# Performance work log

Hardware: AMD Instinct MI355X
Metric: run time of the kernel (lower is better)

The kernel has to match this reference:

```python
import jax, jax.numpy as jnp
import numpy as np

EMBED_DIM = 1024
NUM_HEADS = 16
HEAD_DIM = EMBED_DIM // NUM_HEADS
B, S = 2, 2048


def setup_inputs() -> dict:
    key = jax.random.key(0)
    ks = jax.random.split(key, 11)
    f32 = jnp.float32
    return {
        "q": jax.random.normal(ks[0], (B, S, EMBED_DIM), f32),
        "k": jax.random.normal(ks[1], (B, S, EMBED_DIM), f32),
        "v": jax.random.normal(ks[2], (B, S, EMBED_DIM), f32),
        # per-head projection weights stacked over heads: [H, E, Dh]
        "Wq": jax.random.normal(ks[3], (NUM_HEADS, EMBED_DIM, HEAD_DIM), f32),
        "Wk": jax.random.normal(ks[4], (NUM_HEADS, EMBED_DIM, HEAD_DIM), f32),
        "Wv": jax.random.normal(ks[5], (NUM_HEADS, EMBED_DIM, HEAD_DIM), f32),
        "bq": jax.random.normal(ks[6], (NUM_HEADS, HEAD_DIM), f32),
        "bk": jax.random.normal(ks[7], (NUM_HEADS, HEAD_DIM), f32),
        "bv": jax.random.normal(ks[8], (NUM_HEADS, HEAD_DIM), f32),
        "Wo": jax.random.normal(ks[9], (EMBED_DIM, EMBED_DIM), f32),
        "bo": jax.random.normal(ks[10], (EMBED_DIM,), f32),
    }


def reference(q, k, v, Wq, Wk, Wv, bq, bk, bv, Wo, bo):
    scale = jnp.asarray(np.sqrt(HEAD_DIM), q.dtype)
    # batched per-head projections: [B,S,E] x [H,E,D] -> [B,H,S,D]
    Q = jnp.einsum("bse,hed->bhsd", q, Wq) + bq[None, :, None, :]
    K = jnp.einsum("bse,hed->bhsd", k, Wk) + bk[None, :, None, :]
    V = jnp.einsum("bse,hed->bhsd", v, Wv) + bv[None, :, None, :]
    # attention scores [B,H,S,S]; original applies mask to a discarded tensor,
    # so output is unmasked softmax(QK^T/scale) @ V
    att = jnp.einsum("bhsd,bhtd->bhst", Q, K) / scale
    att = jax.nn.softmax(att, axis=-1)
    ctx = jnp.einsum("bhst,bhtd->bhsd", att, V)  # [B,H,S,D]
    # concat heads (head order preserved) then output projection
    ctx = ctx.transpose(0, 2, 1, 3).reshape(ctx.shape[0], ctx.shape[2], -1)  # [B,S,E]
    return ctx @ Wo + bo
```

## Files before the change

kernel.cpp:

```cpp
#include <hip/hip_runtime.h>
#include <hip/hip_bf16.h>

typedef unsigned short u16;
typedef unsigned int   u32;
typedef _Float16 f16;
typedef __attribute__((ext_vector_type(4))) float f32x4;
typedef __attribute__((ext_vector_type(8))) short s16x8;
typedef __attribute__((ext_vector_type(8))) f16 f16x8;
typedef __attribute__((ext_vector_type(2))) __fp16 fp16x2;
typedef __attribute__((ext_vector_type(4))) u16 u16x4;
typedef __attribute__((ext_vector_type(2))) u32 u32x2;

#define DI __device__ __forceinline__

static constexpr int Bb = 2, Ss = 2048, Hh = 16, Dd = 64, Ee = 1024;
static constexpr int Mrows = Bb * Ss;
static constexpr size_t NE = (size_t)Mrows * Ee;
static constexpr size_t WN = (size_t)Ee * Ee;
static constexpr float QSCALE = 0.125f * 1.44269504088896f;

DI float bf2f(u16 h) { u32 u = ((u32)h) << 16; return __builtin_bit_cast(float, u); }
DI u16 f2bf(float f) {
    u32 u = __builtin_bit_cast(u32, f);
    u32 r = (u + 0x7FFFu + ((u >> 16) & 1u)) >> 16;
    return (u16)r;
}
DI u16 f2h(float f) { f16 h = (f16)f; return __builtin_bit_cast(u16, h); }
DI u32 pkrtz(float a, float b) {
    fp16x2 r = __builtin_amdgcn_cvt_pkrtz(a, b);
    return __builtin_bit_cast(u32, r);
}
DI float ex2(float x) { return __builtin_amdgcn_exp2f(x); }

#define MFMA_BF(a, b, c) __builtin_amdgcn_mfma_f32_16x16x32_bf16((a), (b), (c), 0, 0, 0)
#define MFMA_F16(a, b, c) __builtin_amdgcn_mfma_f32_16x16x32_f16( \
    __builtin_bit_cast(f16x8, (a)), __builtin_bit_cast(f16x8, (b)), (c), 0, 0, 0)

DI void gld16(const u16* g, u16* l) {
    __builtin_amdgcn_global_load_lds((const __attribute__((address_space(1))) void*)g,
                                     (__attribute__((address_space(3))) void*)l, 16, 0, 0);
}

__global__ __launch_bounds__(256) void k_split3(
    const float* __restrict__ q, const float* __restrict__ k, const float* __restrict__ v,
    u16* __restrict__ qh, u16* __restrict__ ql,
    u16* __restrict__ kh, u16* __restrict__ kl, u16* __restrict__ vh) {
    int i = blockIdx.x * 256 + threadIdx.x;
    int y = blockIdx.y;
    if (y == 2) { vh[i] = f2h(v[i]); return; }
    const float* s = y ? k : q;
    u16* h = y ? kh : qh;
    u16* l = y ? kl : ql;
    float val = s[i];
    u16 hh = f2bf(val);
    h[i] = hh;
    l[i] = f2bf(val - bf2f(hh));
}

__global__ __launch_bounds__(256) void k_wprep(
    const float* __restrict__ Wq, const float* __restrict__ Wk,
    const float* __restrict__ Wv, const float* __restrict__ Wo,
    u16* __restrict__ WqTh, u16* __restrict__ WqTl,
    u16* __restrict__ WkTh, u16* __restrict__ WkTl,
    u16* __restrict__ WvT, u16* __restrict__ WoT) {
    __shared__ float Ts[64 * 65];
    const int y = blockIdx.y;
    const int ti = blockIdx.x >> 4, tj = blockIdx.x & 15;
    const float* W = (y == 0) ? Wq : (y == 1) ? Wk : (y == 2) ? Wv : Wo;
    const int t = threadIdx.x;
    const int col = t & 63, rb = (t >> 6) * 16;
#pragma unroll
    for (int rr = 0; rr < 16; rr++) {
        int row = rb + rr;
        float v = (y < 3) ? W[(size_t)ti * 65536 + (size_t)(tj * 64 + row) * 64 + col]
                          : W[(size_t)(tj * 64 + row) * Ee + ti * 64 + col];
        Ts[row * 65 + col] = v;
    }
    __syncthreads();
#pragma unroll
    for (int rr = 0; rr < 16; rr++) {
        int orow = rb + rr;
        int ocol = col;
        float v = Ts[ocol * 65 + orow];
        size_t oidx = (size_t)(ti * 64 + orow) * Ee + tj * 64 + ocol;
        if (y == 0) {
            u16 hh = f2bf(v); WqTh[oidx] = hh; WqTl[oidx] = f2bf(v - bf2f(hh));
        } else if (y == 1) {
            u16 hh = f2bf(v); WkTh[oidx] = hh; WkTl[oidx] = f2bf(v - bf2f(hh));
        } else if (y == 2) {
            WvT[oidx] = f2h(v);
        } else {
            WoT[oidx] = f2h(v);
        }
    }
}

template <int SPLIT, int F16, int OUTMODE>
DI void gemm_body(const u16* __restrict__ Ah, const u16* __restrict__ Al,
                  const u16* __restrict__ Bh, const u16* __restrict__ Bl,
                  const float* __restrict__ bias,
                  u16* __restrict__ C16h, u16* __restrict__ C16l, float* __restrict__ Cf,
                  float scale, u16* As0, u16* As1, u16* Bs0, u16* Bs1) {
    constexpr int M = Mrows, N = Ee, K = Ee;
    const int tid = threadIdx.x;
    const int wave = tid >> 6, lane = tid & 63;
    const int quad = lane >> 4, l16 = lane & 15;
    const int m0 = blockIdx.y * 128, n0 = blockIdx.x * 128;
    const int wm = (wave >> 1) * 64, wn = (wave & 1) * 64;

    f32x4 acc[4][4];
#pragma unroll
    for (int i = 0; i < 4; i++)
#pragma unroll
        for (int j = 0; j < 4; j++) acc[i][j] = (f32x4)0.0f;

    for (int kk = 0; kk < K; kk += 32) {
        __syncthreads();
#pragma unroll
        for (int i = 0; i < 2; i++) {
            int c = tid + i * 256;
            int row = c >> 2, j = c & 3;
            size_t ga = (size_t)(m0 + row) * K + kk + j * 8;
            gld16(Ah + ga, As0 + c * 8);
            if constexpr (SPLIT) gld16(Al + ga, As1 + c * 8);
            size_t gb = (size_t)(n0 + row) * K + kk + j * 8;
            gld16(Bh + gb, Bs0 + c * 8);
            if constexpr (SPLIT) gld16(Bl + gb, Bs1 + c * 8);
        }
        __syncthreads();

        s16x8 bf[4][2];
#pragma unroll
        for (int nt = 0; nt < 4; nt++) {
            int r = wn + nt * 16 + l16;
            bf[nt][0] = *(const s16x8*)&Bs0[r * 32 + quad * 8];
            if constexpr (SPLIT) bf[nt][1] = *(const s16x8*)&Bs1[r * 32 + quad * 8];
        }
#pragma unroll
        for (int mt = 0; mt < 4; mt++) {
            int r = wm + mt * 16 + l16;
            s16x8 a0 = *(const s16x8*)&As0[r * 32 + quad * 8];
            s16x8 a1;
            if constexpr (SPLIT) a1 = *(const s16x8*)&As1[r * 32 + quad * 8];
#pragma unroll
            for (int nt = 0; nt < 4; nt++) {
                if constexpr (F16) {
                    acc[mt][nt] = MFMA_F16(a0, bf[nt][0], acc[mt][nt]);
                } else {
                    acc[mt][nt] = MFMA_BF(a0, bf[nt][0], acc[mt][nt]);
                    if constexpr (SPLIT) {
                        acc[mt][nt] = MFMA_BF(a0, bf[nt][1], acc[mt][nt]);
                        acc[mt][nt] = MFMA_BF(a1, bf[nt][0], acc[mt][nt]);
                    }
                }
            }
        }
    }

#pragma unroll
    for (int mt = 0; mt < 4; mt++)
#pragma unroll
        for (int nt = 0; nt < 4; nt++) {
            int gn = n0 + wn + nt * 16 + l16;
            float bs = bias[gn];
            if constexpr (OUTMODE == 1) {
                int gm = m0 + wm + mt * 16 + quad * 4;
                u16x4 pk;
#pragma unroll
                for (int r = 0; r < 4; r++) pk[r] = f2h((acc[mt][nt][r] + bs) * scale);
                *(u16x4*)&C16h[(size_t)gn * M + gm] = pk;
            } else {
#pragma unroll
                for (int r = 0; r < 4; r++) {
                    int gm = m0 + wm + mt * 16 + quad * 4 + r;
                    float v = (acc[mt][nt][r] + bs) * scale;
                    if constexpr (OUTMODE == 0) {
                        Cf[(size_t)gm * N + gn] = v;
                    } else {
                        u16 hh = f2bf(v);
                        C16h[(size_t)gm * N + gn] = hh;
                        C16l[(size_t)gm * N + gn] = f2bf(v - bf2f(hh));
                    }
                }
            }
        }
}

__global__ __launch_bounds__(256, 3) void k_qkv(
    const u16* __restrict__ qh, const u16* __restrict__ ql,
    const u16* __restrict__ kh, const u16* __restrict__ kl,
    const u16* __restrict__ vh,
    const u16* __restrict__ WqTh, const u16* __restrict__ WqTl,
    const u16* __restrict__ WkTh, const u16* __restrict__ WkTl,
    const u16* __restrict__ WvT,
    const float* __restrict__ bq, const float* __restrict__ bk, const float* __restrict__ bv,
    u16* __restrict__ Qh, u16* __restrict__ Ql2,
    u16* __restrict__ Kh, u16* __restrict__ Kl2, u16* __restrict__ Vt) {
    __shared__ u16 As[2][128 * 32];
    __shared__ u16 Bs[2][128 * 32];
    int z = blockIdx.z;
    if (z == 0)
        gemm_body<1, 0, 2>(qh, ql, WqTh, WqTl, bq, Qh, Ql2, nullptr, QSCALE,
                           As[0], As[1], Bs[0], Bs[1]);
    else if (z == 1)
        gemm_body<1, 0, 2>(kh, kl, WkTh, WkTl, bk, Kh, Kl2, nullptr, 1.0f,
                           As[0], As[1], Bs[0], Bs[1]);
    else
        gemm_body<0, 1, 1>(vh, nullptr, WvT, nullptr, bv, Vt, nullptr, nullptr, 1.0f,
                           As[0], As[1], Bs[0], Bs[1]);
}

__global__ __launch_bounds__(256, 3) void k_out(
    const u16* __restrict__ ctx, const u16* __restrict__ WoT,
    const float* __restrict__ bo, float* __restrict__ out) {
    __shared__ u16 As[128 * 32];
    __shared__ u16 Bs[128 * 32];
    gemm_body<0, 1, 0>(ctx, nullptr, WoT, nullptr, bo, nullptr, nullptr, out, 1.0f,
                       As, nullptr, Bs, nullptr);
}

__global__ __launch_bounds__(256, 2) void k_attn(
    const u16* __restrict__ Qh, const u16* __restrict__ Ql,
    const u16* __restrict__ Kh, const u16* __restrict__ Kl,
    const u16* __restrict__ Vt, u16* __restrict__ ctx) {
    const int bh = blockIdx.x;
    const int b = bh >> 4, h = bh & 15;
    const int q0 = blockIdx.y * 128;
    const int rowBase = b * Ss + q0;
    const int hc = h * 64;

    __shared__ u16 Ks[2][64 * 64];
    __shared__ u16 Vs[64 * 64];
    __shared__ u16 Pw[4][32 * 72];

    const int tid = threadIdx.x;
    const int wave = tid >> 6, lane = tid & 63;
    const int quad = lane >> 4, l16 = lane & 15;

    s16x8 bq[2][2][2];
#pragma unroll
    for (int nt = 0; nt < 2; nt++) {
        int row = rowBase + wave * 32 + nt * 16 + l16;
#pragma unroll
        for (int kc = 0; kc < 2; kc++) {
            bq[nt][kc][0] = *(const s16x8*)(Qh + (size_t)row * Ee + hc + kc * 32 + quad * 8);
            bq[nt][kc][1] = *(const s16x8*)(Ql + (size_t)row * Ee + hc + kc * 32 + quad * 8);
        }
    }

    f32x4 o[2][4];
#pragma unroll
    for (int nt = 0; nt < 2; nt++)
#pragma unroll
        for (int dg = 0; dg < 4; dg++) o[nt][dg] = (f32x4)0.0f;
    float m_[2] = {-1e30f, -1e30f};
    float l_[2] = {0.f, 0.f};

    for (int t0 = 0; t0 < Ss; t0 += 64) {
        const int kRowBase = b * Ss + t0;
        __syncthreads();
#pragma unroll
        for (int i = 0; i < 2; i++) {
            int c = tid + i * 256;
            int row = c >> 3, j = c & 7;
            int sj = j ^ (row & 7);
            *(s16x8*)&Ks[0][row * 64 + sj * 8] =
                *(const s16x8*)(Kh + (size_t)(kRowBase + row) * Ee + hc + j * 8);
            *(s16x8*)&Ks[1][row * 64 + sj * 8] =
                *(const s16x8*)(Kl + (size_t)(kRowBase + row) * Ee + hc + j * 8);
            *(s16x8*)&Vs[row * 64 + sj * 8] =
                *(const s16x8*)(Vt + (size_t)(hc + row) * Mrows + kRowBase + j * 8);
        }
        __syncthreads();

        f32x4 st[2][4];
#pragma unroll
        for (int nt = 0; nt < 2; nt++)
#pragma unroll
            for (int mt = 0; mt < 4; mt++) st[nt][mt] = (f32x4)0.0f;
#pragma unroll
        for (int mt = 0; mt < 4; mt++) {
            int tr = mt * 16 + l16;
#pragma unroll
            for (int kc = 0; kc < 2; kc++) {
                int sj = (kc * 4 + quad) ^ (l16 & 7);
                s16x8 akh = *(const s16x8*)&Ks[0][tr * 64 + sj * 8];
                s16x8 akl = *(const s16x8*)&Ks[1][tr * 64 + sj * 8];
#pragma unroll
                for (int nt = 0; nt < 2; nt++) {
                    st[nt][mt] = MFMA_BF(akh, bq[nt][kc][0], st[nt][mt]);
                    st[nt][mt] = MFMA_BF(akh, bq[nt][kc][1], st[nt][mt]);
                    st[nt][mt] = MFMA_BF(akl, bq[nt][kc][0], st[nt][mt]);
                }
            }
        }

#pragma unroll
        for (int nt = 0; nt < 2; nt++) {
            float t01 = fmaxf(fmaxf(st[nt][0][0], st[nt][0][1]), fmaxf(st[nt][0][2], st[nt][0][3]));
            float t23 = fmaxf(fmaxf(st[nt][1][0], st[nt][1][1]), fmaxf(st[nt][1][2], st[nt][1][3]));
            float t45 = fmaxf(fmaxf(st[nt][2][0], st[nt][2][1]), fmaxf(st[nt][2][2], st[nt][2][3]));
            float t67 = fmaxf(fmaxf(st[nt][3][0], st[nt][3][1]), fmaxf(st[nt][3][2], st[nt][3][3]));
            float tmax = fmaxf(fmaxf(t01, t23), fmaxf(t45, t67));
            tmax = fmaxf(tmax, __shfl_xor(tmax, 16));
            tmax = fmaxf(tmax, __shfl_xor(tmax, 32));
            float mnew = fmaxf(m_[nt], tmax);
            float al = ex2(m_[nt] - mnew);
            m_[nt] = mnew;
            float psum = 0.f;
#pragma unroll
            for (int mt = 0; mt < 4; mt++) {
                float p0 = ex2(st[nt][mt][0] - mnew);
                float p1 = ex2(st[nt][mt][1] - mnew);
                float p2 = ex2(st[nt][mt][2] - mnew);
                float p3 = ex2(st[nt][mt][3] - mnew);
                psum += (p0 + p1) + (p2 + p3);
                u32x2 pk;
                pk[0] = pkrtz(p0, p1);
                pk[1] = pkrtz(p2, p3);
                *(u32x2*)&Pw[wave][(nt * 16 + l16) * 72 + mt * 16 + quad * 4] = pk;
            }
            psum += __shfl_xor(psum, 16);
            psum += __shfl_xor(psum, 32);
            l_[nt] = l_[nt] * al + psum;
#pragma unroll
            for (int dg = 0; dg < 4; dg++) o[nt][dg] *= al;
        }

#pragma unroll
        for (int kc = 0; kc < 2; kc++) {
            s16x8 bp[2];
#pragma unroll
            for (int nt = 0; nt < 2; nt++)
                bp[nt] = *(const s16x8*)&Pw[wave][(nt * 16 + l16) * 72 + kc * 32 + quad * 8];
#pragma unroll
            for (int dg = 0; dg < 4; dg++) {
                int sj = (kc * 4 + quad) ^ (l16 & 7);
                s16x8 av = *(const s16x8*)&Vs[(dg * 16 + l16) * 64 + sj * 8];
#pragma unroll
                for (int nt = 0; nt < 2; nt++) o[nt][dg] = MFMA_F16(av, bp[nt], o[nt][dg]);
            }
        }
    }

#pragma unroll
    for (int nt = 0; nt < 2; nt++) {
        float inv = 1.0f / l_[nt];
        int gm = rowBase + wave * 32 + nt * 16 + l16;
#pragma unroll
        for (int dg = 0; dg < 4; dg++) {
            u32x2 pk;
            pk[0] = pkrtz(o[nt][dg][0] * inv, o[nt][dg][1] * inv);
            pk[1] = pkrtz(o[nt][dg][2] * inv, o[nt][dg][3] * inv);
            *(u32x2*)&ctx[(size_t)gm * Ee + hc + dg * 16 + quad * 4] = pk;
        }
    }
}

extern "C" void kernel_launch(void* const* d_in, const int* in_sizes, int n_in,
                              void* d_out, int out_size, void* d_ws, size_t ws_size,
                              hipStream_t stream) {
    const float* q   = (const float*)d_in[0];
    const float* kin = (const float*)d_in[1];
    const float* v   = (const float*)d_in[2];
    const float* Wq  = (const float*)d_in[3];
    const float* Wk  = (const float*)d_in[4];
    const float* Wv  = (const float*)d_in[5];
    const float* bq  = (const float*)d_in[6];
    const float* bk  = (const float*)d_in[7];
    const float* bv  = (const float*)d_in[8];
    const float* Wo  = (const float*)d_in[9];
    const float* bo  = (const float*)d_in[10];

    u16* ws = (u16*)d_ws;
    u16 *qh = ws,          *ql = ws + NE,     *kh = ws + 2 * NE, *kl = ws + 3 * NE;
    u16 *vh = ws + 4 * NE;
    u16 *Qh = ws + 5 * NE, *Ql = ws + 6 * NE, *Kh = ws + 7 * NE, *Kl = ws + 8 * NE;
    u16 *Vt = ws + 9 * NE, *ctx = ws + 10 * NE;
    u16 *WqTh = ws + 11 * NE;
    u16 *WqTl = WqTh + WN, *WkTh = WqTh + 2 * WN, *WkTl = WqTh + 3 * WN;
    u16 *WvT = WqTh + 4 * WN, *WoT = WqTh + 5 * WN;

    dim3 b256(256);
    k_split3<<<dim3(NE / 256, 3), b256, 0, stream>>>(q, kin, v, qh, ql, kh, kl, vh);
    k_wprep<<<dim3(256, 4), b256, 0, stream>>>(Wq, Wk, Wv, Wo,
                                               WqTh, WqTl, WkTh, WkTl, WvT, WoT);

    k_qkv<<<dim3(8, 32, 3), b256, 0, stream>>>(qh, ql, kh, kl, vh,
                                               WqTh, WqTl, WkTh, WkTl, WvT,
                                               bq, bk, bv, Qh, Ql, Kh, Kl, Vt);

    k_attn<<<dim3(Bb * Hh, Ss / 128), b256, 0, stream>>>(Qh, Ql, Kh, Kl, Vt, ctx);

    k_out<<<dim3(8, 32), b256, 0, stream>>>(ctx, WoT, bo, (float*)d_out);
}
```

Measured before the change: 296.3 us.

## Prefetch next K/V tile into registers during attention compute

The attention loop now issues the global loads for the next K/V tile into registers before computing the current tile, and writes them to shared memory only after the current tile's MFMAs finish. This hides global-load latency behind compute. The change also precomputes the swizzled LDS base pointers and raises wave priority around the MFMA sections with s_setprio. In exchange it needs extra registers for the six prefetched vectors, which could reduce occupancy under launch_bounds(256,2).

```diff
diff --git a/kernel.cpp b/kernel.cpp
--- a/kernel.cpp
+++ b/kernel.cpp
@@ -237,6 +237,40 @@
     const int wave = tid >> 6, lane = tid & 63;
     const int quad = lane >> 4, l16 = lane & 15;
 
+    const int c0 = tid, c1 = tid + 256;
+    const int srow0 = c0 >> 3, sgj0 = c0 & 7;
+    const int srow1 = c1 >> 3, sgj1 = c1 & 7;
+    const int soff0 = srow0 * 64 + (sgj0 ^ (srow0 & 7)) * 8;
+    const int soff1 = srow1 * 64 + (sgj1 ^ (srow1 & 7)) * 8;
+
+    s16x8 rkh0, rkh1, rkl0, rkl1, rv0, rv1;
+    auto loadT = [&](int t0) {
+        const int kRowBase = b * Ss + t0;
+        rkh0 = *(const s16x8*)(Kh + (size_t)(kRowBase + srow0) * Ee + hc + sgj0 * 8);
+        rkl0 = *(const s16x8*)(Kl + (size_t)(kRowBase + srow0) * Ee + hc + sgj0 * 8);
+        rv0  = *(const s16x8*)(Vt + (size_t)(hc + srow0) * Mrows + kRowBase + sgj0 * 8);
+        rkh1 = *(const s16x8*)(Kh + (size_t)(kRowBase + srow1) * Ee + hc + sgj1 * 8);
+        rkl1 = *(const s16x8*)(Kl + (size_t)(kRowBase + srow1) * Ee + hc + sgj1 * 8);
+        rv1  = *(const s16x8*)(Vt + (size_t)(hc + srow1) * Mrows + kRowBase + sgj1 * 8);
+    };
+    auto storeT = [&]() {
+        *(s16x8*)&Ks[0][soff0] = rkh0;
+        *(s16x8*)&Ks[0][soff1] = rkh1;
+        *(s16x8*)&Ks[1][soff0] = rkl0;
+        *(s16x8*)&Ks[1][soff1] = rkl1;
+        *(s16x8*)&Vs[soff0] = rv0;
+        *(s16x8*)&Vs[soff1] = rv1;
+    };
+
+    const int sw0 = ((0 * 4 + quad) ^ (l16 & 7)) * 8;
+    const int sw1 = ((1 * 4 + quad) ^ (l16 & 7)) * 8;
+    const u16* akb0 = &Ks[0][l16 * 64 + sw0];
+    const u16* akb1 = &Ks[0][l16 * 64 + sw1];
+    const u16* avb0 = &Vs[l16 * 64 + sw0];
+    const u16* avb1 = &Vs[l16 * 64 + sw1];
+    u16* pwb = &Pw[wave][l16 * 72 + quad * 4];
+    const u16* pbb = &Pw[wave][l16 * 72 + quad * 8];
+
     s16x8 bq[2][2][2];
 #pragma unroll
     for (int nt = 0; nt < 2; nt++) {
@@ -256,44 +290,37 @@
     float m_[2] = {-1e30f, -1e30f};
     float l_[2] = {0.f, 0.f};
 
+    loadT(0);
+    storeT();
+    __syncthreads();
+
     for (int t0 = 0; t0 < Ss; t0 += 64) {
-        const int kRowBase = b * Ss + t0;
-        __syncthreads();
-#pragma unroll
-        for (int i = 0; i < 2; i++) {
-            int c = tid + i * 256;
-            int row = c >> 3, j = c & 7;
-            int sj = j ^ (row & 7);
-            *(s16x8*)&Ks[0][row * 64 + sj * 8] =
-                *(const s16x8*)(Kh + (size_t)(kRowBase + row) * Ee + hc + j * 8);
-            *(s16x8*)&Ks[1][row * 64 + sj * 8] =
-                *(const s16x8*)(Kl + (size_t)(kRowBase + row) * Ee + hc + j * 8);
-            *(s16x8*)&Vs[row * 64 + sj * 8] =
-                *(const s16x8*)(Vt + (size_t)(hc + row) * Mrows + kRowBase + j * 8);
-        }
-        __syncthreads();
+        const bool more = (t0 + 64) < Ss;
+        if (more) loadT(t0 + 64);
 
         f32x4 st[2][4];
 #pragma unroll
         for (int nt = 0; nt < 2; nt++)
 #pragma unroll
             for (int mt = 0; mt < 4; mt++) st[nt][mt] = (f32x4)0.0f;
+        __builtin_amdgcn_s_setprio(1);
 #pragma unroll
         for (int mt = 0; mt < 4; mt++) {
-            int tr = mt * 16 + l16;
-#pragma unroll
-            for (int kc = 0; kc < 2; kc++) {
-                int sj = (kc * 4 + quad) ^ (l16 & 7);
-                s16x8 akh = *(const s16x8*)&Ks[0][tr * 64 + sj * 8];
-                s16x8 akl = *(const s16x8*)&Ks[1][tr * 64 + sj * 8];
-#pragma unroll
-                for (int nt = 0; nt < 2; nt++) {
-                    st[nt][mt] = MFMA_BF(akh, bq[nt][kc][0], st[nt][mt]);
-                    st[nt][mt] = MFMA_BF(akh, bq[nt][kc][1], st[nt][mt]);
-                    st[nt][mt] = MFMA_BF(akl, bq[nt][kc][0], st[nt][mt]);
-                }
+            s16x8 akh0 = *(const s16x8*)(akb0 + mt * 1024);
+            s16x8 akl0 = *(const s16x8*)(akb0 + mt * 1024 + 4096);
+            s16x8 akh1 = *(const s16x8*)(akb1 + mt * 1024);
+            s16x8 akl1 = *(const s16x8*)(akb1 + mt * 1024 + 4096);
+#pragma unroll
+            for (int nt = 0; nt < 2; nt++) {
+                st[nt][mt] = MFMA_BF(akh0, bq[nt][0][0], st[nt][mt]);
+                st[nt][mt] = MFMA_BF(akh0, bq[nt][0][1], st[nt][mt]);
+                st[nt][mt] = MFMA_BF(akl0, bq[nt][0][0], st[nt][mt]);
+                st[nt][mt] = MFMA_BF(akh1, bq[nt][1][0], st[nt][mt]);
+                st[nt][mt] = MFMA_BF(akh1, bq[nt][1][1], st[nt][mt]);
+                st[nt][mt] = MFMA_BF(akl1, bq[nt][1][0], st[nt][mt]);
             }
         }
+        __builtin_amdgcn_s_setprio(0);
 
 #pragma unroll
         for (int nt = 0; nt < 2; nt++) {
@@ -318,7 +345,7 @@
                 u32x2 pk;
                 pk[0] = pkrtz(p0, p1);
                 pk[1] = pkrtz(p2, p3);
-                *(u32x2*)&Pw[wave][(nt * 16 + l16) * 72 + mt * 16 + quad * 4] = pk;
+                *(u32x2*)(pwb + nt * 1152 + mt * 16) = pk;
             }
             psum += __shfl_xor(psum, 16);
             psum += __shfl_xor(psum, 32);
@@ -327,19 +354,27 @@
             for (int dg = 0; dg < 4; dg++) o[nt][dg] *= al;
         }
 
+        __builtin_amdgcn_s_setprio(1);
 #pragma unroll
         for (int kc = 0; kc < 2; kc++) {
             s16x8 bp[2];
 #pragma unroll
             for (int nt = 0; nt < 2; nt++)
-                bp[nt] = *(const s16x8*)&Pw[wave][(nt * 16 + l16) * 72 + kc * 32 + quad * 8];
+                bp[nt] = *(const s16x8*)(pbb + nt * 1152 + kc * 32);
+            const u16* avb = kc ? avb1 : avb0;
 #pragma unroll
             for (int dg = 0; dg < 4; dg++) {
-                int sj = (kc * 4 + quad) ^ (l16 & 7);
-                s16x8 av = *(const s16x8*)&Vs[(dg * 16 + l16) * 64 + sj * 8];
+                s16x8 av = *(const s16x8*)(avb + dg * 1024);
 #pragma unroll
                 for (int nt = 0; nt < 2; nt++) o[nt][dg] = MFMA_F16(av, bp[nt], o[nt][dg]);
             }
+        }
+        __builtin_amdgcn_s_setprio(0);
+
+        if (more) {
+            __syncthreads();
+            storeT();
+            __syncthreads();
         }
     }
 
```

After: 307.3 us. 1.04x slower.
